# Optimization experiments

Hardware: AMD Instinct MI355X
Metric: run time of the kernel (lower is better)

## Reference

```python
import jax, jax.numpy as jnp
import numpy as np

L, D, V, BS, H, HD, DL = 12, 768, 50257, 1024, 12, 64, 256
B, T = 2, 1024
EPS = 1e-5


def _ln(x, w, b):
    m = jnp.mean(x, axis=-1, keepdims=True)
    v = jnp.mean((x - m) ** 2, axis=-1, keepdims=True)
    return (x - m) * jax.lax.rsqrt(v + EPS) * w + b


def _rope_tables(t_len):
    inv_freq = 1.0 / (10000.0 ** (jnp.arange(0, HD, 2, dtype=jnp.float32) / HD))
    t = jnp.arange(t_len, dtype=jnp.float32)
    freqs = jnp.outer(t, inv_freq)  # [T, HD/2]
    return jnp.cos(freqs), jnp.sin(freqs)


def _apply_rope(x, cos, sin):
    # x: [B, H, T, HD]; cos/sin: [T, HD/2]
    c = jnp.concatenate([cos, cos], axis=-1)[None, None]
    s = jnp.concatenate([sin, sin], axis=-1)[None, None]
    x1, x2 = jnp.split(x, 2, axis=-1)
    rot = jnp.concatenate([-x2, x1], axis=-1)
    return x * c + rot * s


def setup_inputs() -> dict:
    key = jax.random.key(0)
    ks = jax.random.split(key, 16)
    std = 0.02
    n = lambda k, shape: jax.random.normal(k, shape, dtype=jnp.float32) * std
    return {
        'idx': jax.random.randint(ks[0], (B, T), 0, V),
        'wte': n(ks[1], (V, D)),
        'wpe': n(ks[2], (BS, D)),
        'ln1_w': jnp.ones((L, D)), 'ln1_b': jnp.zeros((L, D)),
        'wq_w': n(ks[3], (L, D, H * HD)), 'wq_b': jnp.zeros((L, H * HD)),
        'kva_w': n(ks[4], (L, D, DL)), 'kva_b': jnp.zeros((L, DL)),
        'kvb_w': n(ks[5], (L, DL, 2 * H * HD)), 'kvb_b': jnp.zeros((L, 2 * H * HD)),
        'out_w': n(ks[6], (L, H * HD, D)), 'out_b': jnp.zeros((L, D)),
        'ln2_w': jnp.ones((L, D)), 'ln2_b': jnp.zeros((L, D)),
        'fc_w': n(ks[7], (L, D, 4 * D)), 'fc_b': jnp.zeros((L, 4 * D)),
        'proj_w': n(ks[8], (L, 4 * D, D)), 'proj_b': jnp.zeros((L, D)),
        'lnf_w': jnp.ones((D,)), 'lnf_b': jnp.zeros((D,)),
    }


def _forward(idx, wte, wpe, ln1_w, ln1_b, wq_w, wq_b, kva_w, kva_b, kvb_w, kvb_b,
             out_w, out_b, ln2_w, ln2_b, fc_w, fc_b, proj_w, proj_b, lnf_w, lnf_b):
    b, t = idx.shape
    x = wte[idx] + wpe[:t][None]  # [B,T,D]
    cos, sin = _rope_tables(t)
    scale = 1.0 / np.sqrt(HD)
    causal = jnp.tril(jnp.ones((t, t), dtype=bool))
    for l in range(L):
        h = _ln(x, ln1_w[l], ln1_b[l])
        q = (h @ wq_w[l] + wq_b[l]).reshape(b, t, H, HD).transpose(0, 2, 1, 3)
        kv_latent = h @ kva_w[l] + kva_b[l]  # [B,T,DL] (the cacheable latent)
        kv = (kv_latent @ kvb_w[l] + kvb_b[l]).reshape(b, t, 2, H, HD)
        kv = kv.transpose(2, 0, 3, 1, 4)  # [2,B,H,T,HD]
        k, v = kv[0], kv[1]
        q = _apply_rope(q, cos, sin)
        k = _apply_rope(k, cos, sin)
        scores = jnp.einsum('bhtd,bhsd->bhts', q, k) * scale
        scores = jnp.where(causal[None, None], scores, -jnp.inf)
        probs = jax.nn.softmax(scores, axis=-1)
        attn = jnp.einsum('bhts,bhsd->bhtd', probs, v)
        attn = attn.transpose(0, 2, 1, 3).reshape(b, t, H * HD)
        x = x + attn @ out_w[l] + out_b[l]
        h2 = _ln(x, ln2_w[l], ln2_b[l])
        mlp = jax.nn.gelu(h2 @ fc_w[l] + fc_b[l], approximate=False) @ proj_w[l] + proj_b[l]
        x = x + mlp
    x = _ln(x, lnf_w, lnf_b)
    logits = x @ wte.T  # tied lm_head
    return logits


def reference(idx, wte, wpe, ln1_w, ln1_b, wq_w, wq_b, kva_w, kva_b, kvb_w, kvb_b,
              out_w, out_b, ln2_w, ln2_b, fc_w, fc_b, proj_w, proj_b, lnf_w, lnf_b):
    return _forward(idx, wte, wpe, ln1_w, ln1_b, wq_w, wq_b, kva_w, kva_b, kvb_w,
                    kvb_b, out_w, out_b, ln2_w, ln2_b, fc_w, fc_b, proj_w, proj_b,
                    lnf_w, lnf_b)
```

## Files before the change

### kernel.cpp

```cpp
#include <hip/hip_runtime.h>
#include <cstdint>
#include <cstddef>


typedef unsigned short ushortT;
typedef __bf16 bf16x8 __attribute__((ext_vector_type(8)));
typedef float f32x4 __attribute__((ext_vector_type(4)));
typedef unsigned short us8 __attribute__((ext_vector_type(8)));

#define NHEAD 12
#define T_SEQ 1024

__device__ __forceinline__ float bf2f(unsigned short u) {
    union { unsigned int i; float f; } v; v.i = ((unsigned int)u) << 16; return v.f;
}
__device__ __forceinline__ unsigned short f2bf(float f) {
    union { float f; unsigned int i; } v; v.f = f;
    unsigned int r = v.i + 0x7fffu + ((v.i >> 16) & 1u);
    return (unsigned short)(r >> 16);
}
__device__ __forceinline__ unsigned int pack2(float a, float b) {
    return (unsigned int)f2bf(a) | ((unsigned int)f2bf(b) << 16);
}
__device__ __forceinline__ void gload_lds16(const void* g, void* l) {
    __builtin_amdgcn_global_load_lds((__attribute__((address_space(1))) void*)g,
                                     (__attribute__((address_space(3))) void*)l, 16, 0, 0);
}
template <int N>
__device__ __forceinline__ void wait_vmcnt() {
    if constexpr (N == 8)      asm volatile("s_waitcnt vmcnt(8)" ::: "memory");
    else if constexpr (N == 6) asm volatile("s_waitcnt vmcnt(6)" ::: "memory");
    else if constexpr (N == 4) asm volatile("s_waitcnt vmcnt(4)" ::: "memory");
    else                       asm volatile("s_waitcnt vmcnt(0)" ::: "memory");
}

__global__ void transpose_cvt_kernel(const float* __restrict__ in, ushortT* __restrict__ outp,
                                     int K, int N, int outRowOff, size_t outLS) {
    __shared__ float tile[32][33];
    const int tx = threadIdx.x, ty = threadIdx.y;
    const int n0 = blockIdx.x * 32, k0 = blockIdx.y * 32;
    const float* src = in + (size_t)blockIdx.z * K * N;
#pragma unroll
    for (int j = 0; j < 4; ++j)
        tile[ty + j * 8][tx] = src[(size_t)(k0 + ty + j * 8) * N + n0 + tx];
    __syncthreads();
    ushortT* dst = outp + (size_t)blockIdx.z * outLS;
#pragma unroll
    for (int j = 0; j < 4; ++j)
        dst[(size_t)(outRowOff + n0 + ty + j * 8) * K + k0 + tx] = f2bf(tile[tx][ty + j * 8]);
}

__global__ void cvt_wte_kernel(const float* __restrict__ in, ushortT* __restrict__ outp) {
    size_t i4 = (size_t)blockIdx.x * 256 + threadIdx.x;
    ushort4 o;
    if (i4 < 9649344) {
        float4 v = ((const float4*)in)[i4];
        o.x = f2bf(v.x); o.y = f2bf(v.y); o.z = f2bf(v.z); o.w = f2bf(v.w);
    } else { o.x = 0; o.y = 0; o.z = 0; o.w = 0; }
    ((ushort4*)outp)[i4] = o;
}

__global__ void embed_kernel(const int* __restrict__ idx, const float* __restrict__ wte,
                             const float* __restrict__ wpe, float* __restrict__ x) {
    int i = blockIdx.x * 256 + threadIdx.x;
    int row = i / 768, d = i - row * 768;
    int t = row & 1023;
    x[i] = wte[(size_t)idx[row] * 768 + d] + wpe[(size_t)t * 768 + d];
}

__global__ void rope_tables_kernel(float* __restrict__ cosT, float* __restrict__ sinT) {
    int i = blockIdx.x * 256 + threadIdx.x;
    int t = i >> 5, f = i & 31;
    float invf = exp2f(-(float)f * (13.287712379549449f / 32.0f));
    float ang = (float)t * invf;
    cosT[i] = cosf(ang);
    sinT[i] = sinf(ang);
}

__global__ __launch_bounds__(256) void ln_kernel(const float* __restrict__ x,
                                                 const float* __restrict__ wg,
                                                 const float* __restrict__ bg,
                                                 ushortT* __restrict__ outp) {
    const int row = blockIdx.x, tid = threadIdx.x;
    const float* xr = x + (size_t)row * 768;
    float v0 = xr[tid], v1 = xr[tid + 256], v2 = xr[tid + 512];
    float s = v0 + v1 + v2;
    float ss = v0 * v0 + v1 * v1 + v2 * v2;
#pragma unroll
    for (int off = 32; off >= 1; off >>= 1) {
        s += __shfl_xor(s, off);
        ss += __shfl_xor(ss, off);
    }
    __shared__ float sb[4], ssb[4];
    if ((tid & 63) == 0) { sb[tid >> 6] = s; ssb[tid >> 6] = ss; }
    __syncthreads();
    float S = sb[0] + sb[1] + sb[2] + sb[3];
    float SS = ssb[0] + ssb[1] + ssb[2] + ssb[3];
    const float mean = S * (1.0f / 768.0f);
    float var = SS * (1.0f / 768.0f) - mean * mean;
    const float rs = rsqrtf(var + 1e-5f);
    ushortT* orow = outp + (size_t)row * 768;
    orow[tid]       = f2bf((v0 - mean) * rs * wg[tid]       + bg[tid]);
    orow[tid + 256] = f2bf((v1 - mean) * rs * wg[tid + 256] + bg[tid + 256]);
    orow[tid + 512] = f2bf((v2 - mean) * rs * wg[tid + 512] + bg[tid + 512]);
}

template <int BM, int NF, int NTHR, bool ROPE>
__global__ __launch_bounds__(NTHR) void gemmT(
    const ushortT* __restrict__ A, int lda,
    const ushortT* __restrict__ Bt, int ldb,
    int K, int CS, int Nstore,
    const float* __restrict__ bias0, const float* __restrict__ bias1,
    ushortT* __restrict__ outB0, int ld0,
    ushortT* __restrict__ outB1, int ld1, int mode1,
    const float* __restrict__ resid, float* __restrict__ outF, int ldF,
    int act, const float* __restrict__ cosT, const float* __restrict__ sinT) {
    constexpr int NW = NTHR / 64;
    constexpr int WC = (NTHR == 512) ? 2 : 1;
    constexpr int WR = NW / WC;
    constexpr int WMR = BM / WR;
    constexpr int MF = WMR / 16;
    constexpr int NFh = NF / WC;
    constexpr int ABYTES = BM * 128;
    constexpr int BBYTES = NF * 2048;
    constexpr int BUFB = ABYTES + BBYTES;
    constexpr int A_LOADS = (BM * 8) / NTHR;
    constexpr int B_LOADS = (NF * 128) / NTHR;
    constexpr int S = A_LOADS + B_LOADS;
    __shared__ __align__(16) char lds[2 * BUFB];
    const int tid = threadIdx.x;
    const int w = tid >> 6, lane = tid & 63;
    const int wm = (WC == 2) ? (w >> 1) : w;
    const int wn = (WC == 2) ? (w & 1) : 0;
    const int gx = gridDim.x;
    const int nwg = gx * gridDim.y;
    const int flat = blockIdx.x + gx * blockIdx.y;
    const int xcd = flat & 7, loc = flat >> 3;
    const int qq = nwg >> 3, rr_ = nwg & 7;
    const int swz = (xcd < rr_ ? xcd * (qq + 1) : rr_ * (qq + 1) + (xcd - rr_) * qq) + loc;
    const int m0 = (swz % gx) * BM, n0 = (swz / gx) * NF * 16;
    const int fr = lane & 15, kg = lane >> 4;
    const size_t ldaB = (size_t)lda * 2, ldbB = (size_t)ldb * 2;
    const char* Ab = (const char*)A;
    const char* Bb = (const char*)Bt;
    f32x4 acc[MF][NFh] = {};

    auto stage = [&](int buf, int t) {
        const size_t ktB = (size_t)t << 7;
        char* As_ = lds + buf * BUFB;
        char* Bs_ = As_ + ABYTES;
#pragma unroll
        for (int jj = 0; jj < A_LOADS; ++jj) {
            const int i = tid + jj * NTHR;
            const int r = i >> 3, c = i & 7, cc = c ^ (r & 7);
            gload_lds16(Ab + (size_t)(m0 + r) * ldaB + ktB + cc * 16, As_ + i * 16);
        }
#pragma unroll
        for (int jj = 0; jj < B_LOADS; ++jj) {
            const int i = tid + jj * NTHR;
            const int r = i >> 3, c = i & 7, cc = c ^ (r & 7);
            gload_lds16(Bb + (size_t)(n0 + r) * ldbB + ktB + cc * 16, Bs_ + i * 16);
        }
    };

    const int nk = K >> 6;
    stage(0, 0);
    if (nk > 1) { stage(1, 1); wait_vmcnt<S>(); }
    else        { wait_vmcnt<0>(); }
    __builtin_amdgcn_s_barrier();

    for (int t = 0; t < nk; ++t) {
        const int cur = t & 1;
        const char* As_ = lds + cur * BUFB;
        const char* Bs_ = As_ + ABYTES;
        bf16x8 af[MF][2], bfr[NFh][2];
#pragma unroll
        for (int mf = 0; mf < MF; ++mf) {
            const int row = wm * WMR + mf * 16 + fr;
#pragma unroll
            for (int ks = 0; ks < 2; ++ks)
                af[mf][ks] = *(const bf16x8*)(As_ + row * 128 + (((ks * 4 + kg) ^ (row & 7)) << 4));
        }
#pragma unroll
        for (int nf = 0; nf < NFh; ++nf) {
            const int row = wn * (NFh * 16) + nf * 16 + fr;
#pragma unroll
            for (int ks = 0; ks < 2; ++ks)
                bfr[nf][ks] = *(const bf16x8*)(Bs_ + row * 128 + (((ks * 4 + kg) ^ (row & 7)) << 4));
        }
        if (t + 2 < nk) {
            asm volatile("s_waitcnt lgkmcnt(0)" ::: "memory");
            __builtin_amdgcn_s_barrier();
            stage(cur, t + 2);
        }
#pragma unroll
        for (int ks = 0; ks < 2; ++ks)
#pragma unroll
            for (int nf = 0; nf < NFh; ++nf)
#pragma unroll
                for (int mf = 0; mf < MF; ++mf)
                    acc[mf][nf] = __builtin_amdgcn_mfma_f32_16x16x32_bf16(
                        af[mf][ks], bfr[nf][ks], acc[mf][nf], 0, 0, 0);
        if (t + 1 < nk) {
            if (t + 2 < nk) wait_vmcnt<S>();
            else            wait_vmcnt<0>();
            __builtin_amdgcn_s_barrier();
        }
    }

    if constexpr (ROPE) {
        float vv[NF][4];
#pragma unroll
        for (int nf = 0; nf < NF; ++nf) {
            const int gcol = n0 + nf * 16 + fr;
            float bv = (gcol < CS) ? (bias0 ? bias0[gcol] : 0.0f)
                                   : (bias1 ? bias1[gcol - CS] : 0.0f);
#pragma unroll
            for (int j = 0; j < 4; ++j) vv[nf][j] = acc[0][nf][j] + bv;
        }
        if (n0 < 768) {
#pragma unroll
            for (int j = 0; j < 4; ++j) {
                const int grow = m0 + wm * WMR + kg * 4 + j;
                const int t = grow & 1023;
                const float c0 = cosT[t * 32 + fr],      s0 = sinT[t * 32 + fr];
                const float c1 = cosT[t * 32 + 16 + fr], s1 = sinT[t * 32 + 16 + fr];
#pragma unroll
                for (int base = 0; base < NF; base += 4) {
                    float x1 = vv[base + 0][j], x2 = vv[base + 2][j];
                    vv[base + 0][j] = x1 * c0 - x2 * s0;
                    vv[base + 2][j] = x2 * c0 + x1 * s0;
                    float y1 = vv[base + 1][j], y2 = vv[base + 3][j];
                    vv[base + 1][j] = y1 * c1 - y2 * s1;
                    vv[base + 3][j] = y2 * c1 + y1 * s1;
                }
            }
        }
#pragma unroll
        for (int nf = 0; nf < NF; ++nf) {
            const int gcol = n0 + nf * 16 + fr;
            if (gcol >= Nstore) continue;
#pragma unroll
            for (int j = 0; j < 4; ++j) {
                const int grow = m0 + wm * WMR + kg * 4 + j;
                const float v = vv[nf][j];
                if (gcol < CS) {
                    if (outB0) outB0[(size_t)grow * ld0 + gcol] = f2bf(v);
                } else if (outB1) {
                    if (mode1 == 0) {
                        outB1[(size_t)grow * ld1 + gcol - CS] = f2bf(v);
                    } else {
                        const int bb = grow >> 10, tt = grow & 1023;
                        const int hd = gcol - CS;
                        outB1[((size_t)((bb * 12 + (hd >> 6)) * 64 + (hd & 63)) << 10) + tt] = f2bf(v);
                    }
                }
            }
        }
    } else {
#pragma unroll
        for (int mf = 0; mf < MF; ++mf) {
#pragma unroll
            for (int nf = 0; nf < NFh; ++nf) {
                const int gcol = n0 + wn * (NFh * 16) + nf * 16 + fr;
                if (gcol >= Nstore) continue;
                float bv = 0.0f;
                if (gcol < CS) { if (bias0) bv = bias0[gcol]; }
                else           { if (bias1) bv = bias1[gcol - CS]; }
#pragma unroll
                for (int j = 0; j < 4; ++j) {
                    const int grow = m0 + wm * WMR + mf * 16 + kg * 4 + j;
                    float v = acc[mf][nf][j] + bv;
                    if (resid) v += resid[(size_t)grow * ldF + gcol];
                    if (act) v = 0.5f * v * (1.0f + erff(v * 0.70710678118654752f));
                    if (outF) outF[(size_t)grow * ldF + gcol] = v;
                    if (gcol < CS) {
                        if (outB0) outB0[(size_t)grow * ld0 + gcol] = f2bf(v);
                    } else if (outB1) {
                        if (mode1 == 0) {
                            outB1[(size_t)grow * ld1 + gcol - CS] = f2bf(v);
                        } else {
                            const int bb = grow >> 10, tt = grow & 1023;
                            const int hd = gcol - CS;
                            outB1[((size_t)((bb * 12 + (hd >> 6)) * 64 + (hd & 63)) << 10) + tt] = f2bf(v);
                        }
                    }
                }
            }
        }
    }
}

__global__ __launch_bounds__(256) void attn_mfma(const ushortT* __restrict__ q,
                                                 const ushortT* __restrict__ kbuf,
                                                 const ushortT* __restrict__ vT,
                                                 ushortT* __restrict__ attnb) {
    __shared__ __align__(16) char lds[41472];
    const int tid = threadIdx.x, w = tid >> 6, lane = tid & 63;
    const int fr = lane & 15, kg = lane >> 4;
    const int b = blockIdx.y / NHEAD, h = blockIdx.y % NHEAD;
    const int qb = blockIdx.x * 64;
    const int q0 = qb + w * 16;
    const int nst = (qb >> 6) + 1, diag = qb >> 6;

    const ushortT* qrow = q + ((size_t)(b * 1024 + q0 + fr) * 768 + h * 64);
    const bf16x8 qf0 = *(const bf16x8*)(qrow + kg * 8);
    const bf16x8 qf1 = *(const bf16x8*)(qrow + 32 + kg * 8);

    const char* kgb = (const char*)kbuf + ((size_t)(b * 1024) * 768 + h * 64) * 2;
    const char* vgb = (const char*)vT + ((size_t)(b * 12 + h) * 65536) * 2;
    char* Pw = lds + 32768 + w * 2176 + fr * 136;

    auto stage = [&](int buf, int st) {
#pragma unroll
        for (int jj = 0; jj < 2; ++jj) {
            const int i = tid + jj * 256;
            const int r = i >> 3, c = i & 7, cc = c ^ (r & 7);
            gload_lds16(kgb + (size_t)(st * 64 + r) * 1536 + cc * 16, lds + buf * 8192 + i * 16);
            gload_lds16(vgb + (size_t)r * 2048 + st * 128 + cc * 16, lds + 16384 + buf * 8192 + i * 16);
        }
    };

    float m_r = -1e30f, l_r = 0.0f;
    f32x4 o[4] = {};

    stage(0, 0);
    __syncthreads();
    for (int st = 0; st < nst; ++st) {
        const int cur = st & 1;
        if (st + 1 < nst) stage(cur ^ 1, st + 1);
        const char* Kd = lds + cur * 8192;
        const char* Vd = lds + 16384 + cur * 8192;

        f32x4 sfr[4];
#pragma unroll
        for (int n = 0; n < 4; ++n) {
            const int row = n * 16 + fr;
            bf16x8 k0 = *(const bf16x8*)(Kd + row * 128 + ((kg ^ (row & 7)) << 4));
            bf16x8 k1 = *(const bf16x8*)(Kd + row * 128 + (((4 + kg) ^ (row & 7)) << 4));
            f32x4 sa = {0.0f, 0.0f, 0.0f, 0.0f};
            sa = __builtin_amdgcn_mfma_f32_16x16x32_bf16(k0, qf0, sa, 0, 0, 0);
            sa = __builtin_amdgcn_mfma_f32_16x16x32_bf16(k1, qf1, sa, 0, 0, 0);
            sfr[n] = sa;
        }
        const int qoff = w * 16 + fr;
#pragma unroll
        for (int n = 0; n < 4; ++n)
#pragma unroll
            for (int j = 0; j < 4; ++j) {
                float v = sfr[n][j] * 0.125f;
                if (st == diag && (n * 16 + kg * 4 + j) > qoff) v = -1e30f;
                sfr[n][j] = v;
            }
        float tm = -1e30f;
#pragma unroll
        for (int n = 0; n < 4; ++n)
#pragma unroll
            for (int j = 0; j < 4; ++j) tm = fmaxf(tm, sfr[n][j]);
        tm = fmaxf(tm, __shfl_xor(tm, 16));
        tm = fmaxf(tm, __shfl_xor(tm, 32));
        const float mnew = fmaxf(m_r, tm);
        const float fac = __expf(m_r - mnew);
        m_r = mnew;
        l_r *= fac;
        const float ff0 = __shfl(fac, kg * 4 + 0);
        const float ff1 = __shfl(fac, kg * 4 + 1);
        const float ff2 = __shfl(fac, kg * 4 + 2);
        const float ff3 = __shfl(fac, kg * 4 + 3);
#pragma unroll
        for (int nf = 0; nf < 4; ++nf) {
            o[nf][0] *= ff0; o[nf][1] *= ff1; o[nf][2] *= ff2; o[nf][3] *= ff3;
        }
#pragma unroll
        for (int n = 0; n < 4; ++n) {
            float e0 = __expf(sfr[n][0] - mnew);
            float e1 = __expf(sfr[n][1] - mnew);
            float e2 = __expf(sfr[n][2] - mnew);
            float e3 = __expf(sfr[n][3] - mnew);
            l_r += (e0 + e1) + (e2 + e3);
            uint2 pv;
            pv.x = pack2(e0, e1);
            pv.y = pack2(e2, e3);
            *(uint2*)(Pw + n * 32 + kg * 8) = pv;
        }
#pragma unroll
        for (int ks = 0; ks < 2; ++ks) {
            uint2 a0 = *(const uint2*)(Pw + ks * 64 + kg * 16);
            uint2 a1 = *(const uint2*)(Pw + ks * 64 + kg * 16 + 8);
            union { uint4 u; bf16x8 v; } pa;
            pa.u = make_uint4(a0.x, a0.y, a1.x, a1.y);
#pragma unroll
            for (int nf = 0; nf < 4; ++nf) {
                const int row = nf * 16 + fr;
                bf16x8 vf = *(const bf16x8*)(Vd + row * 128 + (((ks * 4 + kg) ^ (row & 7)) << 4));
                o[nf] = __builtin_amdgcn_mfma_f32_16x16x32_bf16(pa.v, vf, o[nf], 0, 0, 0);
            }
        }
        __syncthreads();
    }

    l_r += __shfl_xor(l_r, 16);
    l_r += __shfl_xor(l_r, 32);
    const float inv = 1.0f / l_r;
    const float iv0 = __shfl(inv, kg * 4 + 0);
    const float iv1 = __shfl(inv, kg * 4 + 1);
    const float iv2 = __shfl(inv, kg * 4 + 2);
    const float iv3 = __shfl(inv, kg * 4 + 3);
#pragma unroll
    for (int nf = 0; nf < 4; ++nf) {
        const size_t base = (size_t)(b * 1024 + q0) * 768 + h * 64 + nf * 16 + fr;
        attnb[base + (size_t)(kg * 4 + 0) * 768] = f2bf(o[nf][0] * iv0);
        attnb[base + (size_t)(kg * 4 + 1) * 768] = f2bf(o[nf][1] * iv1);
        attnb[base + (size_t)(kg * 4 + 2) * 768] = f2bf(o[nf][2] * iv2);
        attnb[base + (size_t)(kg * 4 + 3) * 768] = f2bf(o[nf][3] * iv3);
    }
}

extern "C" void kernel_launch(void* const* d_in, const int* in_sizes, int n_in,
                              void* d_out, int out_size, void* d_ws, size_t ws_size,
                              hipStream_t stream) {
    (void)in_sizes; (void)n_in; (void)out_size; (void)ws_size;
    const int*   idxp   = (const int*)d_in[0];
    const float* wte    = (const float*)d_in[1];
    const float* wpe    = (const float*)d_in[2];
    const float* ln1_w  = (const float*)d_in[3];
    const float* ln1_b  = (const float*)d_in[4];
    const float* wq_w   = (const float*)d_in[5];
    const float* wq_b   = (const float*)d_in[6];
    const float* kva_w  = (const float*)d_in[7];
    const float* kva_b  = (const float*)d_in[8];
    const float* kvb_w  = (const float*)d_in[9];
    const float* kvb_b  = (const float*)d_in[10];
    const float* out_w  = (const float*)d_in[11];
    const float* out_b  = (const float*)d_in[12];
    const float* ln2_w  = (const float*)d_in[13];
    const float* ln2_b  = (const float*)d_in[14];
    const float* fc_w   = (const float*)d_in[15];
    const float* fc_b   = (const float*)d_in[16];
    const float* proj_w = (const float*)d_in[17];
    const float* proj_b = (const float*)d_in[18];
    const float* lnf_w  = (const float*)d_in[19];
    const float* lnf_b  = (const float*)d_in[20];

    char* ws = (char*)d_ws;
    size_t off = 0;
    auto alloc = [&](size_t bytes) -> char* {
        char* p = ws + off;
        off += (bytes + 255) & ~(size_t)255;
        return p;
    };
    ushortT* wqkvaT = (ushortT*)alloc((size_t)12 * 1024 * 768 * 2);
    ushortT* kvbT   = (ushortT*)alloc((size_t)12 * 1536 * 256 * 2);
    ushortT* outT   = (ushortT*)alloc((size_t)12 * 768 * 768 * 2);
    ushortT* fcT    = (ushortT*)alloc((size_t)12 * 3072 * 768 * 2);
    ushortT* projT  = (ushortT*)alloc((size_t)12 * 768 * 3072 * 2);
    ushortT* wteB   = (ushortT*)alloc((size_t)50304 * 768 * 2);
    float* cosT = (float*)alloc((size_t)1024 * 32 * 4);
    float* sinT = (float*)alloc((size_t)1024 * 32 * 4);
    float*   x     = (float*)alloc((size_t)2048 * 768 * 4);
    ushortT* h     = (ushortT*)alloc((size_t)2048 * 768 * 2);
    ushortT* qbuf  = (ushortT*)alloc((size_t)2048 * 768 * 2);
    ushortT* lat   = (ushortT*)alloc((size_t)2048 * 256 * 2);
    ushortT* kvbuf = (ushortT*)alloc((size_t)2048 * 768 * 2);
    ushortT* vTb   = (ushortT*)alloc((size_t)24 * 64 * 1024 * 2);
    ushortT* attnb = (ushortT*)alloc((size_t)2048 * 768 * 2);
    ushortT* fca   = (ushortT*)alloc((size_t)2048 * 3072 * 2);

    const dim3 blkT(32, 8);
    transpose_cvt_kernel<<<dim3(24, 24, 12), blkT, 0, stream>>>(wq_w,  wqkvaT, 768, 768,  0,   (size_t)1024 * 768);
    transpose_cvt_kernel<<<dim3(8,  24, 12), blkT, 0, stream>>>(kva_w, wqkvaT, 768, 256,  768, (size_t)1024 * 768);
    transpose_cvt_kernel<<<dim3(48, 8,  12), blkT, 0, stream>>>(kvb_w, kvbT,   256, 1536, 0,   (size_t)1536 * 256);
    transpose_cvt_kernel<<<dim3(24, 24, 12), blkT, 0, stream>>>(out_w, outT,   768, 768,  0,   (size_t)768 * 768);
    transpose_cvt_kernel<<<dim3(96, 24, 12), blkT, 0, stream>>>(fc_w,  fcT,    768, 3072, 0,   (size_t)3072 * 768);
    transpose_cvt_kernel<<<dim3(24, 96, 12), blkT, 0, stream>>>(proj_w, projT, 3072, 768, 0,   (size_t)768 * 3072);
    cvt_wte_kernel<<<37728, 256, 0, stream>>>(wte, wteB);
    rope_tables_kernel<<<128, 256, 0, stream>>>(cosT, sinT);
    embed_kernel<<<6144, 256, 0, stream>>>(idxp, wte, wpe, x);

    for (int l = 0; l < 12; ++l) {
        ln_kernel<<<2048, 256, 0, stream>>>(x, ln1_w + l * 768, ln1_b + l * 768, h);
        gemmT<64, 8, 256, true><<<dim3(32, 8), 256, 0, stream>>>(
            h, 768, wqkvaT + (size_t)l * 1024 * 768, 768,
            768, 768, 1024, wq_b + l * 768, kva_b + l * 256,
            qbuf, 768, lat, 256, 0, nullptr, nullptr, 0, 0, cosT, sinT);
        gemmT<64, 8, 256, true><<<dim3(32, 12), 256, 0, stream>>>(
            lat, 256, kvbT + (size_t)l * 1536 * 256, 256,
            256, 768, 1536, kvb_b + l * 1536, kvb_b + l * 1536 + 768,
            kvbuf, 768, vTb, 0, 1, nullptr, nullptr, 0, 0, cosT, sinT);
        attn_mfma<<<dim3(16, 24), 256, 0, stream>>>(qbuf, kvbuf, vTb, attnb);
        gemmT<64, 8, 256, false><<<dim3(32, 6), 256, 0, stream>>>(
            attnb, 768, outT + (size_t)l * 768 * 768, 768,
            768, 768, 768, out_b + l * 768, nullptr,
            nullptr, 0, nullptr, 0, 0, x, x, 768, 0, nullptr, nullptr);
        ln_kernel<<<2048, 256, 0, stream>>>(x, ln2_w + l * 768, ln2_b + l * 768, h);
        gemmT<128, 8, 512, false><<<dim3(16, 24), 512, 0, stream>>>(
            h, 768, fcT + (size_t)l * 3072 * 768, 768,
            768, 3072, 3072, fc_b + l * 3072, nullptr,
            fca, 3072, nullptr, 0, 0, nullptr, nullptr, 0, 1, nullptr, nullptr);
        gemmT<64, 8, 256, false><<<dim3(32, 6), 256, 0, stream>>>(
            fca, 3072, projT + (size_t)l * 768 * 3072, 3072,
            3072, 768, 768, proj_b + l * 768, nullptr,
            nullptr, 0, nullptr, 0, 0, x, x, 768, 0, nullptr, nullptr);
    }
    ln_kernel<<<2048, 256, 0, stream>>>(x, lnf_w, lnf_b, h);
    gemmT<128, 8, 512, false><<<dim3(16, 393), 512, 0, stream>>>(
        h, 768, wteB, 768,
        768, 50304, 50257, nullptr, nullptr,
        nullptr, 0, nullptr, 0, 0, nullptr, (float*)d_out, 50257, 0, nullptr, nullptr);
}
```

Before: 2.168 ms.

## Use 2D wave grid in GEMM and enlarge FC and lm_head tiles

Reorganises the GEMM kernel's waves into a 2-row by WC-column grid, so each wave computes a squarer sub-tile with more register-level reuse of the A and B fragments. The RoPE epilogue is rewritten to match the new per-wave layout. The FC GEMM moves to 128x192 tiles and the lm_head GEMM to 256x192 tiles to cut repeated global loads. The price is more LDS per block (about 112 KB for lm_head), more accumulator registers, and fewer blocks in flight, which can lower occupancy.

```diff
diff --git a/kernel.cpp b/kernel.cpp
--- a/kernel.cpp
+++ b/kernel.cpp
@@ -29,7 +29,9 @@
 template <int N>
 __device__ __forceinline__ void wait_vmcnt() {
     if constexpr (N == 8)      asm volatile("s_waitcnt vmcnt(8)" ::: "memory");
+    else if constexpr (N == 7) asm volatile("s_waitcnt vmcnt(7)" ::: "memory");
     else if constexpr (N == 6) asm volatile("s_waitcnt vmcnt(6)" ::: "memory");
+    else if constexpr (N == 5) asm volatile("s_waitcnt vmcnt(5)" ::: "memory");
     else if constexpr (N == 4) asm volatile("s_waitcnt vmcnt(4)" ::: "memory");
     else                       asm volatile("s_waitcnt vmcnt(0)" ::: "memory");
 }
@@ -115,12 +117,11 @@
     ushortT* __restrict__ outB1, int ld1, int mode1,
     const float* __restrict__ resid, float* __restrict__ outF, int ldF,
     int act, const float* __restrict__ cosT, const float* __restrict__ sinT) {
-    constexpr int NW = NTHR / 64;
-    constexpr int WC = (NTHR == 512) ? 2 : 1;
-    constexpr int WR = NW / WC;
-    constexpr int WMR = BM / WR;
+    constexpr int WC = (NTHR == 512) ? 4 : 2;
+    constexpr int WMR = BM / 2;
     constexpr int MF = WMR / 16;
     constexpr int NFh = NF / WC;
+    constexpr int WNh = NFh * 16;
     constexpr int ABYTES = BM * 128;
     constexpr int BBYTES = NF * 2048;
     constexpr int BUFB = ABYTES + BBYTES;
@@ -130,8 +131,7 @@
     __shared__ __align__(16) char lds[2 * BUFB];
     const int tid = threadIdx.x;
     const int w = tid >> 6, lane = tid & 63;
-    const int wm = (WC == 2) ? (w >> 1) : w;
-    const int wn = (WC == 2) ? (w & 1) : 0;
+    const int wm = w / WC, wn = w % WC;
     const int gx = gridDim.x;
     const int nwg = gx * gridDim.y;
     const int flat = blockIdx.x + gx * blockIdx.y;
@@ -183,7 +183,7 @@
         }
 #pragma unroll
         for (int nf = 0; nf < NFh; ++nf) {
-            const int row = wn * (NFh * 16) + nf * 16 + fr;
+            const int row = wn * WNh + nf * 16 + fr;
 #pragma unroll
             for (int ks = 0; ks < 2; ++ks)
                 bfr[nf][ks] = *(const bf16x8*)(Bs_ + row * 128 + (((ks * 4 + kg) ^ (row & 7)) << 4));
@@ -209,60 +209,63 @@
     }
 
     if constexpr (ROPE) {
-        float vv[NF][4];
-#pragma unroll
-        for (int nf = 0; nf < NF; ++nf) {
-            const int gcol = n0 + nf * 16 + fr;
-            float bv = (gcol < CS) ? (bias0 ? bias0[gcol] : 0.0f)
-                                   : (bias1 ? bias1[gcol - CS] : 0.0f);
-#pragma unroll
-            for (int j = 0; j < 4; ++j) vv[nf][j] = acc[0][nf][j] + bv;
-        }
-        if (n0 < 768) {
-#pragma unroll
-            for (int j = 0; j < 4; ++j) {
-                const int grow = m0 + wm * WMR + kg * 4 + j;
-                const int t = grow & 1023;
-                const float c0 = cosT[t * 32 + fr],      s0 = sinT[t * 32 + fr];
-                const float c1 = cosT[t * 32 + 16 + fr], s1 = sinT[t * 32 + 16 + fr];
-#pragma unroll
-                for (int base = 0; base < NF; base += 4) {
-                    float x1 = vv[base + 0][j], x2 = vv[base + 2][j];
-                    vv[base + 0][j] = x1 * c0 - x2 * s0;
-                    vv[base + 2][j] = x2 * c0 + x1 * s0;
-                    float y1 = vv[base + 1][j], y2 = vv[base + 3][j];
-                    vv[base + 1][j] = y1 * c1 - y2 * s1;
-                    vv[base + 3][j] = y2 * c1 + y1 * s1;
+        float vv[MF][4][4];
+#pragma unroll
+        for (int mf = 0; mf < MF; ++mf)
+#pragma unroll
+            for (int nf = 0; nf < 4; ++nf) {
+                const int gcol = n0 + wn * 64 + nf * 16 + fr;
+                float bv = (gcol < CS) ? (bias0 ? bias0[gcol] : 0.0f)
+                                       : (bias1 ? bias1[gcol - CS] : 0.0f);
+#pragma unroll
+                for (int j = 0; j < 4; ++j) vv[mf][nf][j] = acc[mf][nf][j] + bv;
+            }
+        if (n0 + wn * 64 < 768) {
+#pragma unroll
+            for (int mf = 0; mf < MF; ++mf)
+#pragma unroll
+                for (int j = 0; j < 4; ++j) {
+                    const int grow = m0 + wm * WMR + mf * 16 + kg * 4 + j;
+                    const int t = grow & 1023;
+                    const float c0 = cosT[t * 32 + fr],      s0 = sinT[t * 32 + fr];
+                    const float c1 = cosT[t * 32 + 16 + fr], s1 = sinT[t * 32 + 16 + fr];
+                    float x1 = vv[mf][0][j], x2 = vv[mf][2][j];
+                    vv[mf][0][j] = x1 * c0 - x2 * s0;
+                    vv[mf][2][j] = x2 * c0 + x1 * s0;
+                    float y1 = vv[mf][1][j], y2 = vv[mf][3][j];
+                    vv[mf][1][j] = y1 * c1 - y2 * s1;
+                    vv[mf][3][j] = y2 * c1 + y1 * s1;
                 }
-            }
-        }
-#pragma unroll
-        for (int nf = 0; nf < NF; ++nf) {
-            const int gcol = n0 + nf * 16 + fr;
-            if (gcol >= Nstore) continue;
-#pragma unroll
-            for (int j = 0; j < 4; ++j) {
-                const int grow = m0 + wm * WMR + kg * 4 + j;
-                const float v = vv[nf][j];
-                if (gcol < CS) {
-                    if (outB0) outB0[(size_t)grow * ld0 + gcol] = f2bf(v);
-                } else if (outB1) {
-                    if (mode1 == 0) {
-                        outB1[(size_t)grow * ld1 + gcol - CS] = f2bf(v);
-                    } else {
-                        const int bb = grow >> 10, tt = grow & 1023;
-                        const int hd = gcol - CS;
-                        outB1[((size_t)((bb * 12 + (hd >> 6)) * 64 + (hd & 63)) << 10) + tt] = f2bf(v);
+        }
+#pragma unroll
+        for (int mf = 0; mf < MF; ++mf)
+#pragma unroll
+            for (int nf = 0; nf < 4; ++nf) {
+                const int gcol = n0 + wn * 64 + nf * 16 + fr;
+                if (gcol >= Nstore) continue;
+#pragma unroll
+                for (int j = 0; j < 4; ++j) {
+                    const int grow = m0 + wm * WMR + mf * 16 + kg * 4 + j;
+                    const float v = vv[mf][nf][j];
+                    if (gcol < CS) {
+                        if (outB0) outB0[(size_t)grow * ld0 + gcol] = f2bf(v);
+                    } else if (outB1) {
+                        if (mode1 == 0) {
+                            outB1[(size_t)grow * ld1 + gcol - CS] = f2bf(v);
+                        } else {
+                            const int bb = grow >> 10, tt = grow & 1023;
+                            const int hd = gcol - CS;
+                            outB1[((size_t)((bb * 12 + (hd >> 6)) * 64 + (hd & 63)) << 10) + tt] = f2bf(v);
+                        }
                     }
                 }
             }
-        }
     } else {
 #pragma unroll
         for (int mf = 0; mf < MF; ++mf) {
 #pragma unroll
             for (int nf = 0; nf < NFh; ++nf) {
-                const int gcol = n0 + wn * (NFh * 16) + nf * 16 + fr;
+                const int gcol = n0 + wn * WNh + nf * 16 + fr;
                 if (gcol >= Nstore) continue;
                 float bv = 0.0f;
                 if (gcol < CS) { if (bias0) bv = bias0[gcol]; }
@@ -493,7 +496,7 @@
             768, 768, 768, out_b + l * 768, nullptr,
             nullptr, 0, nullptr, 0, 0, x, x, 768, 0, nullptr, nullptr);
         ln_kernel<<<2048, 256, 0, stream>>>(x, ln2_w + l * 768, ln2_b + l * 768, h);
-        gemmT<128, 8, 512, false><<<dim3(16, 24), 512, 0, stream>>>(
+        gemmT<128, 12, 512, false><<<dim3(16, 16), 512, 0, stream>>>(
             h, 768, fcT + (size_t)l * 3072 * 768, 768,
             768, 3072, 3072, fc_b + l * 3072, nullptr,
             fca, 3072, nullptr, 0, 0, nullptr, nullptr, 0, 1, nullptr, nullptr);
@@ -503,7 +506,7 @@
             nullptr, 0, nullptr, 0, 0, x, x, 768, 0, nullptr, nullptr);
     }
     ln_kernel<<<2048, 256, 0, stream>>>(x, lnf_w, lnf_b, h);
-    gemmT<128, 8, 512, false><<<dim3(16, 393), 512, 0, stream>>>(
+    gemmT<256, 12, 512, false><<<dim3(8, 262), 512, 0, stream>>>(
         h, 768, wteB, 768,
         768, 50304, 50257, nullptr, nullptr,
         nullptr, 0, nullptr, 0, 0, nullptr, (float*)d_out, 50257, 0, nullptr, nullptr);
```

After: 2.189 ms. Within noise of the previous version (+1.0%).
